# Optimization experiments

Hardware: AMD Instinct MI355X
Metric: run time of the kernel (lower is better)

## Reference

```python
import jax, jax.numpy as jnp
import numpy as np

N, T, D = 2, 2048, 1024
H, HW = 16, 64  # num_heads, head_width
NEG = -1e9


def setup_inputs() -> dict:
    key = jax.random.key(0)
    kx, kq, kk, kv = jax.random.split(key, 4)
    x = jax.random.normal(kx, (N, T, D), dtype=jnp.float32)
    # additive causal mask: 0 on/below diagonal, large negative above
    causal = jnp.triu(jnp.ones((T, T), dtype=jnp.float32), k=1) * NEG
    mask = causal[None, None]  # [1,1,T,T]
    s = 1.0 / np.sqrt(D)
    Wq = jax.random.normal(kq, (D, D), dtype=jnp.float32) * s
    Wk = jax.random.normal(kk, (D, D), dtype=jnp.float32) * s
    Wv = jax.random.normal(kv, (D, D), dtype=jnp.float32) * s
    return {"x": x, "mask": mask, "Wq": Wq, "Wk": Wk, "Wv": Wv}


def _alibi_bias(t):
    # slopes: 2^(-i*8/H) for i = 1..H, shape [H,1,1]
    step = 8.0 / H
    slopes = 2.0 ** (-step * jnp.arange(1, H + 1, dtype=jnp.float32))
    rel = (jnp.arange(t)[None, :] - jnp.arange(t)[:, None]).astype(jnp.float32)  # [t,t], rel[i,j]=j-i
    return slopes[:, None, None] * rel[None]  # [H,t,t]


def reference(x, mask, Wq, Wk, Wv):
    n, t, d = x.shape

    def heads(w):
        # nn.Linear: x @ W^T, then split into heads -> [n,H,t,HW]
        return (x @ w.T).reshape(n, t, H, HW).transpose(0, 2, 1, 3)

    q, k, v = heads(Wq), heads(Wk), heads(Wv)
    att = jnp.einsum("bhqd,bhkd->bhqk", q, k) / np.sqrt(HW)
    att = att + _alibi_bias(t)[None] + mask[:, :, :t, :t]
    att = jax.nn.softmax(att, axis=-1)
    res = jnp.einsum("bhqk,bhkd->bhqd", att, v)
    return res.transpose(0, 2, 1, 3).reshape(n, t, d)
```

## Files before the change

### kernel.cpp

```cpp
#include <hip/hip_runtime.h>
#include <stdint.h>

#define N_B 2
#define T_SEQ 2048
#define D_MODEL 1024
#define N_HEADS 16
#define HEAD_W 64

typedef __attribute__((ext_vector_type(8))) short short8;
typedef __attribute__((ext_vector_type(4))) float f32x4;

#define GLOAD_LDS16(gp, lp)                                                          \
    __builtin_amdgcn_global_load_lds((__attribute__((address_space(1))) void*)(gp),  \
                                     (__attribute__((address_space(3))) void*)(lp),  \
                                     16, 0, 0)

__device__ __forceinline__ unsigned short f2bf(float f) {
    union { float f; uint32_t u; } cv; cv.f = f;
    return (unsigned short)((cv.u + 0x7fffu + ((cv.u >> 16) & 1u)) >> 16);
}

__device__ __forceinline__ uint32_t cvt_pk_bf16(float lo, float hi) {
    uint32_t r;
    asm("v_cvt_pk_bf16_f32 %0, %1, %2" : "=v"(r) : "v"(lo), "v"(hi));
    return r;
}

__device__ __forceinline__ float bf2f(uint32_t us) {
    union { uint32_t u; float f; } cv; cv.u = us << 16; return cv.f;
}

#define LOG2E 1.44269504f

__global__ __launch_bounds__(256) void cvt_fused(const float4* __restrict__ x,
                                                 const float4* __restrict__ wq,
                                                 const float4* __restrict__ wk,
                                                 const float4* __restrict__ wv,
                                                 uint64_t* __restrict__ xb,
                                                 uint64_t* __restrict__ wqb,
                                                 uint64_t* __restrict__ wkb,
                                                 uint64_t* __restrict__ wvb) {
    const int i = blockIdx.x * 256 + threadIdx.x;
    const float4* src; uint64_t* dst; float scale; int off;
    if (i < 1048576)      { src = x;  dst = xb;  scale = 1.f;            off = i; }
    else if (i < 1310720) { src = wq; dst = wqb; scale = 0.125f * LOG2E; off = i - 1048576; }
    else if (i < 1572864) { src = wk; dst = wkb; scale = 1.f;            off = i - 1310720; }
    else                  { src = wv; dst = wvb; scale = 1.f;            off = i - 1572864; }
    float4 v = src[off];
    union { unsigned short us[4]; uint64_t u64; } o;
    o.us[0] = f2bf(v.x * scale);
    o.us[1] = f2bf(v.y * scale);
    o.us[2] = f2bf(v.z * scale);
    o.us[3] = f2bf(v.w * scale);
    dst[off] = o.u64;
}

__global__ __launch_bounds__(256) void qkv_gemm(const unsigned short* __restrict__ A,
                                                const unsigned short* __restrict__ W0,
                                                const unsigned short* __restrict__ W1,
                                                const unsigned short* __restrict__ W2,
                                                unsigned short* __restrict__ O0,
                                                unsigned short* __restrict__ O1,
                                                unsigned short* __restrict__ O2) {
    __shared__ union {
        struct { unsigned short A[128 * 64]; unsigned short W[128 * 64]; } st;
        unsigned short vb[4][64 * 72];
    } sh;
    const int bid0 = blockIdx.x;
    const int bid = (bid0 & 7) * 96 + (bid0 >> 3);
    const int z = bid >> 8;
    const int rem = bid & 255;
    const int m0 = (rem >> 3) * 128;
    const int n0 = (rem & 7) * 128;
    const unsigned short* W = (z == 0) ? W0 : (z == 1) ? W1 : W2;
    const int tid = threadIdx.x;
    const int lane = tid & 63;
    const int ww = tid >> 6;
    const int wr = (ww >> 1) * 64;
    const int wc = (ww & 1) * 64;
    const int g = lane >> 4;
    const int fr = lane & 15;
    const int srow = lane >> 3;
    const int sgr = (lane & 7) ^ srow;

    f32x4 acc[4][4];
#pragma unroll
    for (int i = 0; i < 4; ++i)
#pragma unroll
        for (int j = 0; j < 4; ++j) acc[i][j] = (f32x4){0.f, 0.f, 0.f, 0.f};

    for (int k0 = 0; k0 < D_MODEL; k0 += 64) {
#pragma unroll
        for (int it = 0; it < 4; ++it) {
            const int chunk = ww * 4 + it;
            const int row = chunk * 8 + srow;
            GLOAD_LDS16(A + (size_t)(m0 + row) * D_MODEL + k0 + sgr * 8,
                        (unsigned short*)sh.st.A + chunk * 512);
            GLOAD_LDS16(W + (size_t)(n0 + row) * D_MODEL + k0 + sgr * 8,
                        (unsigned short*)sh.st.W + chunk * 512);
        }
        __syncthreads();
#pragma unroll
        for (int kb = 0; kb < 2; ++kb) {
            short8 af[4], bf[4];
#pragma unroll
            for (int mi = 0; mi < 4; ++mi) {
                const int row = wr + mi * 16 + fr;
                af[mi] = *(const short8*)(sh.st.A + row * 64 +
                                          (((kb * 4 + g) ^ (fr & 7)) * 8));
            }
#pragma unroll
            for (int ni = 0; ni < 4; ++ni) {
                const int row = wc + ni * 16 + fr;
                bf[ni] = *(const short8*)(sh.st.W + row * 64 +
                                          (((kb * 4 + g) ^ (fr & 7)) * 8));
            }
#pragma unroll
            for (int mi = 0; mi < 4; ++mi)
#pragma unroll
                for (int ni = 0; ni < 4; ++ni)
                    acc[mi][ni] = __builtin_amdgcn_mfma_f32_16x16x32_bf16(af[mi], bf[ni],
                                                                          acc[mi][ni], 0, 0, 0);
        }
        __syncthreads();
    }

    const int ro = g * 4;
    if (z < 2) {
        unsigned short* outp = (z == 0) ? O0 : O1;
#pragma unroll
        for (int mi = 0; mi < 4; ++mi) {
#pragma unroll
            for (int ni = 0; ni < 4; ++ni) {
#pragma unroll
                for (int r = 0; r < 4; ++r) {
                    const int m = m0 + wr + mi * 16 + ro + r;
                    const int n = n0 + wc + ni * 16 + fr;
                    const int b = m >> 11, t = m & (T_SEQ - 1);
                    const int h = n >> 6, wd = n & (HEAD_W - 1);
                    outp[((size_t)(b * N_HEADS + h) * T_SEQ + t) * HEAD_W + wd] =
                        f2bf(acc[mi][ni][r]);
                }
            }
        }
    } else {
#pragma unroll
        for (int mi = 0; mi < 4; ++mi)
#pragma unroll
            for (int ni = 0; ni < 4; ++ni)
#pragma unroll
                for (int r = 0; r < 4; ++r)
                    sh.vb[ww][(ni * 16 + fr) * 72 + mi * 16 + ro + r] = f2bf(acc[mi][ni][r]);
#pragma unroll
        for (int rep = 0; rep < 8; ++rep) {
            const int nl = rep * 8 + (lane >> 3);
            const int n = n0 + wc + nl;
            const int h = n >> 6, wd = n & (HEAD_W - 1);
            const int m = m0 + wr + (lane & 7) * 8;
            const int b = m >> 11, t = m & (T_SEQ - 1);
            short8 vv = *(const short8*)(&sh.vb[ww][nl * 72 + (lane & 7) * 8]);
            *(short8*)(O2 + ((size_t)(b * N_HEADS + h) * HEAD_W + wd) * T_SEQ + t) = vv;
        }
    }
}

__global__ __launch_bounds__(256, 5) void attn_fwd(const unsigned short* __restrict__ Qb,
                                                   const unsigned short* __restrict__ Kb,
                                                   const unsigned short* __restrict__ Vtb,
                                                   float* __restrict__ outp,
                                                   unsigned short* __restrict__ opart,
                                                   float* __restrict__ lpart) {
    __shared__ unsigned short Kl[2][64 * 64];
    __shared__ unsigned short Vl[2][64 * 64];

    const int bid = blockIdx.x;
    int ib, ck;
    if (bid < 1024)      { ck = 0; ib = bid; }
    else if (bid < 1536) { ck = 1; ib = bid - 1024; }
    else                 { ck = 2; ib = bid - 1536; }
    const int qi = 31 - (ib >> 5);
    const int b = (ib >> 4) & 1;
    const int h = ((ib & 15) + 5 * (ib >> 8)) & 15;
    const int q0 = qi * 64;
    const int tid = threadIdx.x, lane = tid & 63, w = tid >> 6;
    const int qw = q0 + w * 16;
    const float slope2 = exp2f(-0.5f * (float)(h + 1)) * LOG2E;

    const float tlf = ((float)q0 - 63.0f - 40.0f / slope2) * 0.015625f;
    const int t_lo = (tlf > 0.0f) ? (int)ceilf(tlf) : 0;

    const bool deep = (qi >= 16);
    const bool single = !deep || (t_lo > qi - 16);
    int t_start, t_end;
    if (ck == 0) {
        t_start = qi;
        t_end = single ? t_lo : (qi - 15);
    } else if (ck == 1) {
        t_start = qi - 16;
        t_end = (t_lo > qi - 23) ? t_lo : (qi - 23);
        if (t_start < t_end) return;
    } else {
        t_start = qi - 24;
        t_end = t_lo;
        if (t_start < t_end) return;
    }
    const int slot = (((qi - 16) << 5) | (h << 1) | b) + (ck << 9);

    const unsigned short* Qp = Qb + (size_t)(b * N_HEADS + h) * T_SEQ * HEAD_W;
    const unsigned short* Kp = Kb + (size_t)(b * N_HEADS + h) * T_SEQ * HEAD_W;
    const unsigned short* Vp = Vtb + (size_t)(b * N_HEADS + h) * HEAD_W * T_SEQ;

    const int g = lane >> 4, c = lane & 15;
    const int srow = lane >> 3;
    const int sgr = (lane & 7) ^ srow;
    const bool ghi = (g >= 2);

#define STAGE_KV(buf, k0_)                                                               \
    {                                                                                    \
        _Pragma("unroll")                                                                \
        for (int it = 0; it < 2; ++it) {                                                 \
            const int ch = w * 2 + it;                                                   \
            const int row = ch * 8 + srow;                                               \
            GLOAD_LDS16(Kp + (size_t)((k0_) + row) * HEAD_W + sgr * 8,                   \
                        (unsigned short*)Kl[buf] + ch * 512);                            \
            GLOAD_LDS16(Vp + (size_t)row * T_SEQ + (k0_) + sgr * 8,                      \
                        (unsigned short*)Vl[buf] + ch * 512);                            \
        }                                                                                \
    }

    short8 qf[2];
#pragma unroll
    for (int kb = 0; kb < 2; ++kb)
        qf[kb] = *(const short8*)(Qp + (size_t)(qw + c) * HEAD_W + kb * 32 + g * 8);

    float K16[4][4];
#pragma unroll
    for (int ct = 0; ct < 4; ++ct)
#pragma unroll
        for (int r = 0; r < 4; ++r)
            K16[ct][r] = slope2 * (float)(ct * 16 + g * 4 + r - qw - c) - 30.0f;

    union { uint32_t u[4]; short8 s8; } one_u;
#pragma unroll
    for (int i = 0; i < 4; ++i) one_u.u[i] = 0x3F803F80u;
    const short8 ones8 = one_u.s8;

    f32x4 o[4];
#pragma unroll
    for (int i = 0; i < 4; ++i) o[i] = (f32x4){0.f, 0.f, 0.f, 0.f};
    f32x4 lac = (f32x4){0.f, 0.f, 0.f, 0.f};

    STAGE_KV(t_start & 1, t_start * 64);
    __syncthreads();

    for (int t = t_start; t >= t_end; --t) {
        const int k0 = t * 64;
        if (t > t_end) STAGE_KV((t - 1) & 1, k0 - 64);
        const unsigned short* Kt = Kl[t & 1];
        const unsigned short* Vt = Vl[t & 1];

        f32x4 s[4];
#pragma unroll
        for (int ct = 0; ct < 4; ++ct) s[ct] = (f32x4){0.f, 0.f, 0.f, 0.f};
#pragma unroll
        for (int ct = 0; ct < 4; ++ct)
#pragma unroll
            for (int kb = 0; kb < 2; ++kb) {
                const short8 kf = *(const short8*)(Kt + (ct * 16 + c) * 64 +
                                                   (((kb * 4 + g) ^ (c & 7)) * 8));
                s[ct] = __builtin_amdgcn_mfma_f32_16x16x32_bf16(kf, qf[kb], s[ct], 0, 0, 0);
            }

        if (t == qi) {
            const int ri = w * 16 + c - g * 4;
#pragma unroll
            for (int ct = 0; ct < 4; ++ct)
#pragma unroll
                for (int r = 0; r < 4; ++r)
                    s[ct][r] = (ct * 16 + r > ri) ? -1e30f : s[ct][r];
        }

        const float ut = slope2 * (float)k0;
        uint32_t pk[4][2];
#pragma unroll
        for (int ct = 0; ct < 4; ++ct) {
            float p[4];
#pragma unroll
            for (int r = 0; r < 4; ++r)
                p[r] = exp2f(s[ct][r] + K16[ct][r] + ut);
            pk[ct][0] = cvt_pk_bf16(p[0], p[1]);
            pk[ct][1] = cvt_pk_bf16(p[2], p[3]);
        }

#pragma unroll
        for (int kb = 0; kb < 2; ++kb) {
            uint32_t pu[4];
#pragma unroll
            for (int v = 0; v < 2; ++v) {
                const uint32_t s0v = ghi ? pk[2 * kb + 1][v] : pk[2 * kb][v];
                const uint32_t s1v = ghi ? pk[2 * kb][v]     : pk[2 * kb + 1][v];
                const uint32_t x16 = __shfl_xor(s0v, 16);
                const uint32_t x32 = __shfl_xor(s1v, 32);
                const uint32_t x48 = __shfl_xor(s1v, 48);
                pu[v]     = (g == 0) ? s0v : (g == 1) ? x48 : (g == 2) ? x32 : x16;
                pu[2 + v] = (g == 0) ? x16 : (g == 1) ? x32 : (g == 2) ? x48 : s0v;
            }
            union { uint32_t u[4]; short8 s8; } pa;
            pa.u[0] = pu[0]; pa.u[1] = pu[1]; pa.u[2] = pu[2]; pa.u[3] = pu[3];
#pragma unroll
            for (int db = 0; db < 4; ++db) {
                const short8 vf = *(const short8*)(Vt + (db * 16 + c) * 64 +
                                                   (((kb * 4 + g) ^ (c & 7)) * 8));
                o[db] = __builtin_amdgcn_mfma_f32_16x16x32_bf16(pa.s8, vf, o[db], 0, 0, 0);
            }
            lac = __builtin_amdgcn_mfma_f32_16x16x32_bf16(pa.s8, ones8, lac, 0, 0, 0);
        }
        __syncthreads();
    }

    if (single) {
        float linv[4];
#pragma unroll
        for (int r = 0; r < 4; ++r) linv[r] = 1.0f / lac[r];
#pragma unroll
        for (int db = 0; db < 4; ++db)
#pragma unroll
            for (int r = 0; r < 4; ++r)
                outp[((size_t)b * T_SEQ + qw + g * 4 + r) * D_MODEL + h * HEAD_W + db * 16 + c] =
                    o[db][r] * linv[r];
    } else {
        uint64_t* op64 = (uint64_t*)(opart + (size_t)slot * 4096 + tid * 16);
#pragma unroll
        for (int db = 0; db < 4; ++db) {
            const uint32_t lo = cvt_pk_bf16(o[db][0], o[db][1]);
            const uint32_t hi = cvt_pk_bf16(o[db][2], o[db][3]);
            op64[db] = (uint64_t)lo | ((uint64_t)hi << 32);
        }
        if (c == 0)
            *(f32x4*)(lpart + slot * 64 + w * 16 + g * 4) = lac;
    }
#undef STAGE_KV
}

__global__ __launch_bounds__(256) void attn_reduce(const unsigned short* __restrict__ opart,
                                                   const float* __restrict__ lpart,
                                                   float* __restrict__ outp) {
    const int slot = blockIdx.x;
    const int qi = 16 + (slot >> 5);
    const int h = (slot & 31) >> 1;
    const int b = slot & 1;
    const float slope2 = exp2f(-0.5f * (float)(h + 1)) * LOG2E;
    const int q0 = qi * 64;
    const float tlf = ((float)q0 - 63.0f - 40.0f / slope2) * 0.015625f;
    const int t_lo = (tlf > 0.0f) ? (int)ceilf(tlf) : 0;
    if (t_lo > qi - 16) return;
    const bool has1b = (t_lo <= qi - 24);

    const int tid = threadIdx.x, lane = tid & 63, w = tid >> 6;
    const int g = lane >> 4, c = lane & 15;
    const int rowb = w * 16 + g * 4;

    const uint64_t* p0 = (const uint64_t*)(opart + (size_t)slot * 4096 + tid * 16);
    const uint64_t* p1 = (const uint64_t*)(opart + (size_t)(slot + 512) * 4096 + tid * 16);
    const uint64_t* p2 = (const uint64_t*)(opart + (size_t)(slot + 1024) * 4096 + tid * 16);

    float linv[4];
#pragma unroll
    for (int r = 0; r < 4; ++r) {
        float lsum = lpart[slot * 64 + rowb + r] + lpart[(slot + 512) * 64 + rowb + r];
        if (has1b) lsum += lpart[(slot + 1024) * 64 + rowb + r];
        linv[r] = 1.0f / lsum;
    }

#pragma unroll
    for (int db = 0; db < 4; ++db) {
        const uint64_t a = p0[db];
        const uint64_t bb = p1[db];
        const uint64_t cc = has1b ? p2[db] : 0ull;
#pragma unroll
        for (int r = 0; r < 4; ++r) {
            float s = bf2f((uint32_t)((a >> (16 * r)) & 0xFFFFu)) +
                      bf2f((uint32_t)((bb >> (16 * r)) & 0xFFFFu));
            if (has1b) s += bf2f((uint32_t)((cc >> (16 * r)) & 0xFFFFu));
            outp[((size_t)b * T_SEQ + q0 + rowb + r) * D_MODEL + h * HEAD_W + db * 16 + c] =
                s * linv[r];
        }
    }
}

extern "C" void kernel_launch(void* const* d_in, const int* in_sizes, int n_in,
                              void* d_out, int out_size, void* d_ws, size_t ws_size,
                              hipStream_t stream) {
    const float* x  = (const float*)d_in[0];
    const float* Wq = (const float*)d_in[2];
    const float* Wk = (const float*)d_in[3];
    const float* Wv = (const float*)d_in[4];
    float* out = (float*)d_out;

    uint8_t* ws = (uint8_t*)d_ws;
    unsigned short* xb  = (unsigned short*)(ws);
    unsigned short* wqb = (unsigned short*)(ws + 8388608);
    unsigned short* wkb = (unsigned short*)(ws + 10485760);
    unsigned short* wvb = (unsigned short*)(ws + 12582912);
    unsigned short* Qb  = (unsigned short*)(ws + 14680064);
    unsigned short* Kb  = (unsigned short*)(ws + 23068672);
    unsigned short* Vtb = (unsigned short*)(ws + 31457280);
    unsigned short* opart = (unsigned short*)(ws);
    float*          lpart = (float*)(ws + 12582912);

    cvt_fused<<<7168, 256, 0, stream>>>((const float4*)x, (const float4*)Wq,
                                        (const float4*)Wk, (const float4*)Wv,
                                        (uint64_t*)xb, (uint64_t*)wqb,
                                        (uint64_t*)wkb, (uint64_t*)wvb);

    qkv_gemm<<<768, 256, 0, stream>>>(xb, wqb, wkb, wvb, Qb, Kb, Vtb);

    attn_fwd<<<2048, 256, 0, stream>>>(Qb, Kb, Vtb, out, opart, lpart);
    attn_reduce<<<512, 256, 0, stream>>>(opart, lpart, out);
}
```

Before: 91.61 us.

## Split attention KV range into finer chunks of 8 tiles for better load balance

Reworks the split-KV scheme so each query tile's key range is cut into chunks of at most 8 key tiles (up to four partials) instead of 16 plus 8, and also splits mid-depth query tiles. The grid grows to 3072 attention blocks and 640 reduce blocks, with a new slot layout for partial outputs and row sums. This aims to shorten the longest per-block critical path and balance work across CUs. In exchange it adds more partial writes, more reduce traffic and extra bf16 rounding of partials.

```diff
diff --git a/kernel.cpp b/kernel.cpp
--- a/kernel.cpp
+++ b/kernel.cpp
@@ -177,7 +177,9 @@
     int ib, ck;
     if (bid < 1024)      { ck = 0; ib = bid; }
     else if (bid < 1536) { ck = 1; ib = bid - 1024; }
-    else                 { ck = 2; ib = bid - 1536; }
+    else if (bid < 2048) { ck = 1; ib = 512 + (bid - 1536); }
+    else if (bid < 2560) { ck = 2; ib = bid - 2048; }
+    else                 { ck = 3; ib = bid - 2560; }
     const int qi = 31 - (ib >> 5);
     const int b = (ib >> 4) & 1;
     const int h = ((ib & 15) + 5 * (ib >> 8)) & 15;
@@ -190,21 +192,34 @@
     const int t_lo = (tlf > 0.0f) ? (int)ceilf(tlf) : 0;
 
     const bool deep = (qi >= 16);
-    const bool single = !deep || (t_lo > qi - 16);
-    int t_start, t_end;
+    const int key32   = ((qi - 16) << 5) | (h << 1) | b;
+    const int key16_4 = ((qi - 16) << 4) | ((h & 7) << 1) | b;
+    const int key24_4 = ((qi - 24) << 4) | ((h & 7) << 1) | b;
+    const int key8_4  = ((qi - 8) << 4) | ((h & 7) << 1) | b;
+
+    bool single = false;
+    int t_start, t_end, slot = 0;
     if (ck == 0) {
         t_start = qi;
-        t_end = single ? t_lo : (qi - 15);
+        single = (t_lo > qi - 8);
+        t_end = single ? t_lo : (qi - 7);
+        if (!single) slot = deep ? key32 : (1152 + key8_4);
     } else if (ck == 1) {
+        if (t_lo > qi - 8) return;
+        t_start = qi - 8;
+        t_end = deep ? ((t_lo > qi - 15) ? t_lo : (qi - 15)) : t_lo;
+        slot = deep ? (512 + key16_4) : (1280 + key8_4);
+    } else if (ck == 2) {
+        if (t_lo > qi - 16) return;
         t_start = qi - 16;
         t_end = (t_lo > qi - 23) ? t_lo : (qi - 23);
-        if (t_start < t_end) return;
+        slot = 768 + key16_4;
     } else {
+        if (t_lo > qi - 24) return;
         t_start = qi - 24;
         t_end = t_lo;
-        if (t_start < t_end) return;
-    }
-    const int slot = (((qi - 16) << 5) | (h << 1) | b) + (ck << 9);
+        slot = 1024 + key24_4;
+    }
 
     const unsigned short* Qp = Qb + (size_t)(b * N_HEADS + h) * T_SEQ * HEAD_W;
     const unsigned short* Kp = Kb + (size_t)(b * N_HEADS + h) * T_SEQ * HEAD_W;
@@ -345,30 +360,49 @@
 __global__ __launch_bounds__(256) void attn_reduce(const unsigned short* __restrict__ opart,
                                                    const float* __restrict__ lpart,
                                                    float* __restrict__ outp) {
-    const int slot = blockIdx.x;
-    const int qi = 16 + (slot >> 5);
-    const int h = (slot & 31) >> 1;
-    const int b = slot & 1;
+    const int bid = blockIdx.x;
+    int qi, h, b;
+    bool deep;
+    if (bid < 512) {
+        deep = true;
+        qi = 16 + (bid >> 5); h = (bid & 31) >> 1; b = bid & 1;
+    } else {
+        deep = false;
+        const int i = bid - 512;
+        qi = 8 + (i >> 4); h = 8 + ((i >> 1) & 7); b = i & 1;
+    }
     const float slope2 = exp2f(-0.5f * (float)(h + 1)) * LOG2E;
     const int q0 = qi * 64;
     const float tlf = ((float)q0 - 63.0f - 40.0f / slope2) * 0.015625f;
     const int t_lo = (tlf > 0.0f) ? (int)ceilf(tlf) : 0;
-    if (t_lo > qi - 16) return;
-    const bool has1b = (t_lo <= qi - 24);
+    if (t_lo > qi - 8) return;
+
+    const int key32   = ((qi - 16) << 5) | (h << 1) | b;
+    const int key16_4 = ((qi - 16) << 4) | ((h & 7) << 1) | b;
+    const int key24_4 = ((qi - 24) << 4) | ((h & 7) << 1) | b;
+    const int key8_4  = ((qi - 8) << 4) | ((h & 7) << 1) | b;
+    const int s0 = deep ? key32 : (1152 + key8_4);
+    const int s1 = deep ? (512 + key16_4) : (1280 + key8_4);
+    const bool has2 = deep && (t_lo <= qi - 16);
+    const bool has3 = deep && (t_lo <= qi - 24);
+    const int s2 = 768 + key16_4;
+    const int s3 = 1024 + key24_4;
 
     const int tid = threadIdx.x, lane = tid & 63, w = tid >> 6;
     const int g = lane >> 4, c = lane & 15;
     const int rowb = w * 16 + g * 4;
 
-    const uint64_t* p0 = (const uint64_t*)(opart + (size_t)slot * 4096 + tid * 16);
-    const uint64_t* p1 = (const uint64_t*)(opart + (size_t)(slot + 512) * 4096 + tid * 16);
-    const uint64_t* p2 = (const uint64_t*)(opart + (size_t)(slot + 1024) * 4096 + tid * 16);
+    const uint64_t* p0 = (const uint64_t*)(opart + (size_t)s0 * 4096 + tid * 16);
+    const uint64_t* p1 = (const uint64_t*)(opart + (size_t)s1 * 4096 + tid * 16);
+    const uint64_t* p2 = (const uint64_t*)(opart + (size_t)s2 * 4096 + tid * 16);
+    const uint64_t* p3 = (const uint64_t*)(opart + (size_t)s3 * 4096 + tid * 16);
 
     float linv[4];
 #pragma unroll
     for (int r = 0; r < 4; ++r) {
-        float lsum = lpart[slot * 64 + rowb + r] + lpart[(slot + 512) * 64 + rowb + r];
-        if (has1b) lsum += lpart[(slot + 1024) * 64 + rowb + r];
+        float lsum = lpart[s0 * 64 + rowb + r] + lpart[s1 * 64 + rowb + r];
+        if (has2) lsum += lpart[s2 * 64 + rowb + r];
+        if (has3) lsum += lpart[s3 * 64 + rowb + r];
         linv[r] = 1.0f / lsum;
     }
 
@@ -376,12 +410,14 @@
     for (int db = 0; db < 4; ++db) {
         const uint64_t a = p0[db];
         const uint64_t bb = p1[db];
-        const uint64_t cc = has1b ? p2[db] : 0ull;
+        const uint64_t cc = has2 ? p2[db] : 0ull;
+        const uint64_t dd = has3 ? p3[db] : 0ull;
 #pragma unroll
         for (int r = 0; r < 4; ++r) {
             float s = bf2f((uint32_t)((a >> (16 * r)) & 0xFFFFu)) +
                       bf2f((uint32_t)((bb >> (16 * r)) & 0xFFFFu));
-            if (has1b) s += bf2f((uint32_t)((cc >> (16 * r)) & 0xFFFFu));
+            if (has2) s += bf2f((uint32_t)((cc >> (16 * r)) & 0xFFFFu));
+            if (has3) s += bf2f((uint32_t)((dd >> (16 * r)) & 0xFFFFu));
             outp[((size_t)b * T_SEQ + q0 + rowb + r) * D_MODEL + h * HEAD_W + db * 16 + c] =
                 s * linv[r];
         }
@@ -406,7 +442,7 @@
     unsigned short* Kb  = (unsigned short*)(ws + 23068672);
     unsigned short* Vtb = (unsigned short*)(ws + 31457280);
     unsigned short* opart = (unsigned short*)(ws);
-    float*          lpart = (float*)(ws + 12582912);
+    float*          lpart = (float*)(ws + 11534336);
 
     cvt_fused<<<7168, 256, 0, stream>>>((const float4*)x, (const float4*)Wq,
                                         (const float4*)Wk, (const float4*)Wv,
@@ -415,6 +451,6 @@
 
     qkv_gemm<<<768, 256, 0, stream>>>(xb, wqb, wkb, wvb, Qb, Kb, Vtb);
 
-    attn_fwd<<<2048, 256, 0, stream>>>(Qb, Kb, Vtb, out, opart, lpart);
-    attn_reduce<<<512, 256, 0, stream>>>(opart, lpart, out);
-}
+    attn_fwd<<<3072, 256, 0, stream>>>(Qb, Kb, Vtb, out, opart, lpart);
+    attn_reduce<<<640, 256, 0, stream>>>(opart, lpart, out);
+}
```

Measured after the change: 96.56 us. +5.4%, slower.
